# Kernel tuning notes

Hardware: AMD Instinct MI355X
Metric: run time of the kernel (lower is better)

The kernel has to match this reference:

```python
import jax, jax.numpy as jnp
import numpy as np

B, S, D, H, FB, K, FC = 16, 512, 256, 8, 128, 64, 32


def setup_inputs() -> dict:
    key = jax.random.key(0)
    ks = jax.random.split(key, 16)
    g = lambda i, shp: jax.random.normal(ks[i], shp, dtype=jnp.float32)
    inp = {
        "B_target": g(0, (B, S, FB)),
        "B_infected": g(1, (B, S, FB)),
        "E_target": g(2, (B, S, D)),
        "E_infected": g(3, (B, S, D)),
        "C_target": jax.random.uniform(ks[4], (B, S, K, FC), dtype=jnp.float32),
        "C_infected": jax.random.uniform(ks[5], (B, S, K, FC), dtype=jnp.float32),
        # learned parameters
        "W_bs": g(6, (FB, 1)) * 0.1,
        "W_cs": g(7, (FC, 1)) * 0.1,
        "W1": g(8, (H, D, D)) * (1.0 / np.sqrt(D)),  # per-head Attn W1, batched
        "W2": g(9, (H, D, D)) * (1.0 / np.sqrt(D)),
        "gamma_bs": jnp.ones((S,), jnp.float32),
        "beta_bs": jnp.zeros((S,), jnp.float32),
        "gamma_cs": jnp.ones((S,), jnp.float32),
        "beta_cs": jnp.zeros((S,), jnp.float32),
        "W_f": g(10, (2, 1)) * 0.1,
    }
    return inp


def _weighted_sum(x, W):
    # tf.nn.softmax over trailing size-1 axis of [F,1] -> all ones (faithful)
    return jnp.squeeze(x @ jax.nn.softmax(W, axis=-1), -1)


def _l2norm(x):
    return x * jax.lax.rsqrt(jnp.maximum(jnp.sum(x * x, -1, keepdims=True), 1e-12))


def _layernorm(x, gamma, beta, eps=1e-16):
    m = jnp.mean(x, -1, keepdims=True)
    v = jnp.mean(jnp.square(x - m), -1, keepdims=True)
    return (x - m) * jax.lax.rsqrt(v + eps) * gamma + beta


def _kld(y_true, y_pred, eps=1e-7):
    yt = jnp.clip(y_true, eps, 1.0)
    yp = jnp.clip(y_pred, eps, 1.0)
    return jnp.sum(yt * jnp.log(yt / yp), -1)


def _attn_br(Bvec, E, W1, W2):
    # batched multi-head version of the per-head Attn loop
    Q = jnp.einsum('bsd,hde->bhse', E, W1)
    Kh = jnp.einsum('bsd,hde->bhse', E, W2)
    scale = 1.0 / jnp.sqrt(jnp.asarray(E.shape[-1], E.dtype))
    scores = jnp.einsum('bhse,bhte->bhst', Q, Kh) * scale  # [b,H,S,S]
    A = jax.nn.softmax(scores, axis=2)  # original softmax(axis=1) on [b,S,S]
    # Dot(axes=(1,1)) of [b,S] with [b,S,S] -> [b,S]; stack heads, transpose -> [b,S,H]
    return jnp.einsum('bs,bhst->bth', Bvec, A)


def reference(B_target, B_infected, E_target, E_infected, C_target, C_infected,
              W_bs, W_cs, W1, W2, gamma_bs, beta_bs, gamma_cs, beta_cs, W_f):
    Bt = _weighted_sum(B_target, W_bs)   # [b,S]
    Bi = _weighted_sum(B_infected, W_bs)
    BR_t = _attn_br(Bt, E_target, W1, W2)    # [b,S,H]
    BR_i = _attn_br(Bi, E_infected, W1, W2)
    # keras CosineSimilarity loss = -cos_sim
    cos = -jnp.sum(_l2norm(BR_i) * _l2norm(BR_t), -1)  # [b,S]
    BS_out = _layernorm(cos, gamma_bs, beta_bs)
    Ct = _weighted_sum(C_target, W_cs)   # [b,S,K]
    Ci = _weighted_sum(C_infected, W_cs)
    Cm = 0.5 * (Ct + Ci)
    Cv = 0.5 * _kld(Ci, Cm) + 0.5 * _kld(Ct, Cm)  # [b,S]
    CS_out = _layernorm(Cv, gamma_cs, beta_cs)
    composite = jnp.stack([BS_out, CS_out], axis=-1)  # [b,S,2]
    out = jnp.squeeze(composite @ jax.nn.softmax(W_f, axis=-1), -1)
    return (out, BS_out, CS_out)
```

## Files before the change

kernel.cpp:

```cpp
#include <hip/hip_runtime.h>

#define NB 16
#define NS 512
#define ND 256
#define NH 8
#define NFB 128
#define NK 64
#define NFC 32

using f16 = _Float16;
using f16x4 = __attribute__((ext_vector_type(4))) f16;
using f16x8 = __attribute__((ext_vector_type(8))) f16;
using f32x4 = __attribute__((ext_vector_type(4))) float;

__device__ inline float waveReduceSum(float v) {
    #pragma unroll
    for (int off = 32; off; off >>= 1) v += __shfl_down(v, off);
    return v;
}

__device__ inline f32x4 mfma16(f16x8 a, f16x8 b, f32x4 c) {
    return __builtin_amdgcn_mfma_f32_16x16x32_f16(a, b, c, 0, 0, 0);
}

__global__ __launch_bounds__(256) void k_prep(const float* __restrict__ W1, const float* __restrict__ W2,
                                              f16* __restrict__ Mth,
                                              const float* __restrict__ Et_in, const float* __restrict__ Ei_in,
                                              f16* __restrict__ Ot, f16* __restrict__ Oi,
                                              const float* __restrict__ Bt_in, const float* __restrict__ Bi_in,
                                              float* __restrict__ Bt, float* __restrict__ Bi,
                                              const float* __restrict__ Ct, const float* __restrict__ Ci,
                                              float* __restrict__ Cv) {
    __shared__ float Wa[64][36];
    __shared__ float Wb[64][36];
    int bid = blockIdx.x;
    int tid = threadIdx.x;

    if (bid < 128) {
        int h  = bid >> 4;
        int j0 = ((bid >> 2) & 3) * 64;
        int i0 = (bid & 3) * 64;
        const float* A  = W2 + (size_t)h * ND * ND;
        const float* Bm = W1 + (size_t)h * ND * ND;
        int r = tid >> 4, c = tid & 15;
        float acc[4][4] = {};
        for (int d0 = 0; d0 < ND; d0 += 32) {
            __syncthreads();
            #pragma unroll
            for (int i = 0; i < 2; ++i) {
                int sid = tid + i * 256;
                int row = sid >> 3, seg = sid & 7;
                *(float4*)&Wa[row][seg * 4] = *(const float4*)&A [(size_t)(j0 + row) * ND + d0 + seg * 4];
                *(float4*)&Wb[row][seg * 4] = *(const float4*)&Bm[(size_t)(i0 + row) * ND + d0 + seg * 4];
            }
            __syncthreads();
            #pragma unroll 8
            for (int d = 0; d < 32; ++d) {
                float a0 = Wa[r*4+0][d], a1 = Wa[r*4+1][d], a2 = Wa[r*4+2][d], a3 = Wa[r*4+3][d];
                float b0 = Wb[c*4+0][d], b1 = Wb[c*4+1][d], b2 = Wb[c*4+2][d], b3 = Wb[c*4+3][d];
                acc[0][0] += a0*b0; acc[0][1] += a0*b1; acc[0][2] += a0*b2; acc[0][3] += a0*b3;
                acc[1][0] += a1*b0; acc[1][1] += a1*b1; acc[1][2] += a1*b2; acc[1][3] += a1*b3;
                acc[2][0] += a2*b0; acc[2][1] += a2*b1; acc[2][2] += a2*b2; acc[2][3] += a2*b3;
                acc[3][0] += a3*b0; acc[3][1] += a3*b1; acc[3][2] += a3*b2; acc[3][3] += a3*b3;
            }
        }
        #pragma unroll
        for (int a = 0; a < 4; ++a)
            #pragma unroll
            for (int bb = 0; bb < 4; ++bb)
                Mth[(size_t)h * ND * ND + (size_t)(j0 + r * 4 + a) * ND + (i0 + c * 4 + bb)] = (f16)acc[a][bb];
    } else if (bid < 128 + 4096) {
        const int n4 = NB * NS * ND / 4;
        int i = (bid - 128) * 256 + tid;
        const float* src; f16* dst;
        if (i < n4) { src = Et_in; dst = Ot; }
        else        { src = Ei_in; dst = Oi; i -= n4; }
        float4 v = ((const float4*)src)[i];
        f16x4 o = { (f16)v.x, (f16)v.y, (f16)v.z, (f16)v.w };
        ((f16x4*)dst)[i] = o;
    } else if (bid < 128 + 8192) {
        int wid = ((bid - 128 - 4096) * 256 + tid) >> 6;
        int lane = tid & 63;
        const float* src; float* dst; int row;
        if (wid < NB * NS) { src = Bt_in; dst = Bt; row = wid; }
        else               { src = Bi_in; dst = Bi; row = wid - NB * NS; }
        float2 v = ((const float2*)(src + (size_t)row * NFB))[lane];
        float s = waveReduceSum(v.x + v.y);
        if (lane == 0) dst[row] = s;
    } else {
        int gw = ((bid - 128 - 8192) * 256 + tid) >> 6;
        int lane = tid & 63;
        const float* pt = Ct + ((size_t)gw * NK + lane) * NFC;
        const float* pi = Ci + ((size_t)gw * NK + lane) * NFC;
        float st = 0.f, si = 0.f;
        #pragma unroll
        for (int j = 0; j < NFC; j += 4) {
            float4 vt = *(const float4*)(pt + j); st += vt.x + vt.y + vt.z + vt.w;
            float4 vi = *(const float4*)(pi + j); si += vi.x + vi.y + vi.z + vi.w;
        }
        float cm = 0.5f * (st + si);
        float yp = fminf(fmaxf(cm, 1e-7f), 1.0f);
        float y1 = fminf(fmaxf(si, 1e-7f), 1.0f);
        float y2 = fminf(fmaxf(st, 1e-7f), 1.0f);
        float term = 0.5f * (y1 * logf(y1 / yp) + y2 * logf(y2 / yp));
        term = waveReduceSum(term);
        if (lane == 0) Cv[gw] = term;
    }
}

__global__ __launch_bounds__(256, 2)
void k_attn4(const f16* __restrict__ Eft, const f16* __restrict__ Efi,
             const f16* __restrict__ Mth,
             const float* __restrict__ Bst, const float* __restrict__ Bsi,
             float* __restrict__ PEt, float* __restrict__ PBt,
             float* __restrict__ PEi, float* __restrict__ PBi) {
    int x = blockIdx.x;
    const f16* E; const float* Bvg; float *PE, *PB;
    if (x < 512) { E = Eft; Bvg = Bst; PE = PEt; PB = PBt; }
    else         { x -= 512; E = Efi; Bvg = Bsi; PE = PEi; PB = PBi; }
    int b = x >> 5, h = (x >> 2) & 7;
    int s0 = (x & 3) * 128;
    const f16* Ebase = E + (size_t)b * NS * ND;
    const f16* Mh = Mth + (size_t)h * ND * ND;
    float* PEo = PE + (size_t)(b * NH + h) * NS;
    float* PBo = PB + (size_t)(b * NH + h) * NS;

    __shared__ f16 smem[2 * 64 * 264];
    __shared__ float pe_s[NS], pb_s[NS];

    int tid = threadIdx.x;
    int lane = tid & 63, w = tid >> 6;
    int l16 = lane & 15, ch = lane >> 4;

    pe_s[tid] = 0.f; pe_s[tid + 256] = 0.f;
    pb_s[tid] = 0.f; pb_s[tid + 256] = 0.f;

    int sw0 = s0 + w * 32;

    f16x8 af[2][8];
    #pragma unroll
    for (int st = 0; st < 2; ++st) {
        f16x8 ebf[8];
        #pragma unroll
        for (int ki = 0; ki < 8; ++ki)
            ebf[ki] = *(const f16x8*)&Ebase[(size_t)(sw0 + st * 16 + l16) * ND + ki * 32 + ch * 8];

        #pragma unroll
        for (int jc = 0; jc < 8; ++jc) {
            __syncthreads();
            #pragma unroll
            for (int it = 0; it < 4; ++it) {
                int sid = tid + it * 256;
                int row = sid >> 5, seg = sid & 31;
                *(int4*)&smem[row * 264 + seg * 8] = *(const int4*)&Mh[(size_t)(jc * 32 + row) * ND + seg * 8];
            }
            __syncthreads();
            f32x4 acc[2] = {};
            #pragma unroll
            for (int ki = 0; ki < 8; ++ki) {
                f16x8 a0 = *(const f16x8*)&smem[(l16)      * 264 + ki * 32 + ch * 8];
                f16x8 a1 = *(const f16x8*)&smem[(16 + l16) * 264 + ki * 32 + ch * 8];
                acc[0] = mfma16(a0, ebf[ki], acc[0]);
                acc[1] = mfma16(a1, ebf[ki], acc[1]);
            }
            f16x8 vv;
            #pragma unroll
            for (int r = 0; r < 4; ++r) { vv[r] = (f16)acc[0][r]; vv[4 + r] = (f16)acc[1][r]; }
            af[st][jc] = vv;
        }
    }
    __syncthreads();

    float bvr[2][4];
    #pragma unroll
    for (int st = 0; st < 2; ++st)
        #pragma unroll
        for (int r = 0; r < 4; ++r)
            bvr[st][r] = Bvg[b * NS + sw0 + st * 16 + 4 * ch + r];

    int4 v[8];
    #pragma unroll
    for (int i = 0; i < 8; ++i) {
        int sid = tid + i * 256;
        int row = sid >> 5, seg = sid & 31;
        v[i] = *(const int4*)&Ebase[(size_t)row * ND + seg * 8];
    }
    #pragma unroll
    for (int i = 0; i < 8; ++i) {
        int sid = tid + i * 256;
        int row = sid >> 5, seg = sid & 31;
        *(int4*)&smem[row * 264 + seg * 8] = v[i];
    }

    for (int t = 0; t < 8; ++t) {
        f16* cur = smem + (t & 1) * (64 * 264);
        f16* nxt = smem + ((t + 1) & 1) * (64 * 264);
        if (t < 7) {
            int t0n = (t + 1) * 64;
            #pragma unroll
            for (int i = 0; i < 8; ++i) {
                int sid = tid + i * 256;
                int row = sid >> 5, seg = sid & 31;
                v[i] = *(const int4*)&Ebase[(size_t)(t0n + row) * ND + seg * 8];
            }
        }
        __syncthreads();
        int t0 = t * 64;
        f32x4 sacc[2][4] = {};
        #pragma unroll
        for (int kk = 0; kk < 8; ++kk)
            #pragma unroll
            for (int nt = 0; nt < 4; ++nt) {
                const f16* ep = &cur[(nt * 16 + l16) * 264 + kk * 32 + 4 * ch];
                f16x4 lo = *(const f16x4*)ep;
                f16x4 hi = *(const f16x4*)(ep + 16);
                f16x8 bf = { lo[0], lo[1], lo[2], lo[3], hi[0], hi[1], hi[2], hi[3] };
                sacc[0][nt] = mfma16(af[0][kk], bf, sacc[0][nt]);
                sacc[1][nt] = mfma16(af[1][kk], bf, sacc[1][nt]);
            }
        if (t < 7) {
            #pragma unroll
            for (int i = 0; i < 8; ++i) {
                int sid = tid + i * 256;
                int row = sid >> 5, seg = sid & 31;
                *(int4*)&nxt[row * 264 + seg * 8] = v[i];
            }
        }
        #pragma unroll
        for (int nt = 0; nt < 4; ++nt) {
            float se = 0.f, sw = 0.f;
            #pragma unroll
            for (int st = 0; st < 2; ++st)
                #pragma unroll
                for (int r = 0; r < 4; ++r) {
                    float e = __expf(sacc[st][nt][r] * 0.0625f);
                    se += e; sw += bvr[st][r] * e;
                }
            se += __shfl_down(se, 32); se += __shfl_down(se, 16);
            sw += __shfl_down(sw, 32); sw += __shfl_down(sw, 16);
            if (ch == 0) {
                atomicAdd(&pe_s[t0 + nt * 16 + l16], se);
                atomicAdd(&pb_s[t0 + nt * 16 + l16], sw);
            }
        }
    }
    __syncthreads();
    atomicAdd(&PEo[tid],       pe_s[tid]);
    atomicAdd(&PEo[tid + 256], pe_s[tid + 256]);
    atomicAdd(&PBo[tid],       pb_s[tid]);
    atomicAdd(&PBo[tid + 256], pb_s[tid + 256]);
}

__device__ inline float blockSum512(float v, float* rbuf) {
    v = waveReduceSum(v);
    int lane = threadIdx.x & 63, w = threadIdx.x >> 6;
    __syncthreads();
    if (lane == 0) rbuf[w] = v;
    __syncthreads();
    float s = 0.f;
    #pragma unroll
    for (int i = 0; i < 8; ++i) s += rbuf[i];
    return s;
}

__global__ __launch_bounds__(512) void k_final(const float* __restrict__ PEt, const float* __restrict__ PBt,
                                               const float* __restrict__ PEi, const float* __restrict__ PBi,
                                               const float* __restrict__ Cv,
                                               const float* __restrict__ gbs, const float* __restrict__ bbs,
                                               const float* __restrict__ gcs, const float* __restrict__ bcs,
                                               float* __restrict__ out) {
    __shared__ float rbuf[8];
    int b = blockIdx.x, s = threadIdx.x;
    float dot = 0.f, nt = 0.f, nu = 0.f;
    #pragma unroll
    for (int h = 0; h < NH; ++h) {
        size_t idx = (size_t)(b * NH + h) * NS + s;
        float tv = PBt[idx] / PEt[idx];
        float iv = PBi[idx] / PEi[idx];
        dot += tv * iv; nt += tv * tv; nu += iv * iv;
    }
    float cosv = -(dot * rsqrtf(fmaxf(nt, 1e-12f)) * rsqrtf(fmaxf(nu, 1e-12f)));

    float mc = blockSum512(cosv, rbuf) * (1.f / 512.f);
    float dc = cosv - mc;
    float vc = blockSum512(dc * dc, rbuf) * (1.f / 512.f);
    float BS = dc * rsqrtf(vc + 1e-16f) * gbs[s] + bbs[s];

    float cv = Cv[(size_t)b * NS + s];
    float mv = blockSum512(cv, rbuf) * (1.f / 512.f);
    float dv = cv - mv;
    float vv = blockSum512(dv * dv, rbuf) * (1.f / 512.f);
    float CS = dv * rsqrtf(vv + 1e-16f) * gcs[s] + bcs[s];

    out[(size_t)b * NS + s] = BS + CS;
    out[(size_t)NB * NS + (size_t)b * NS + s] = BS;
    out[(size_t)2 * NB * NS + (size_t)b * NS + s] = CS;
}

extern "C" void kernel_launch(void* const* d_in, const int* in_sizes, int n_in,
                              void* d_out, int out_size, void* d_ws, size_t ws_size,
                              hipStream_t stream) {
    const float* B_target   = (const float*)d_in[0];
    const float* B_infected = (const float*)d_in[1];
    const float* E_target   = (const float*)d_in[2];
    const float* E_infected = (const float*)d_in[3];
    const float* C_target   = (const float*)d_in[4];
    const float* C_infected = (const float*)d_in[5];
    const float* W1  = (const float*)d_in[8];
    const float* W2  = (const float*)d_in[9];
    const float* gbs = (const float*)d_in[10];
    const float* bbs = (const float*)d_in[11];
    const float* gcs = (const float*)d_in[12];
    const float* bcs = (const float*)d_in[13];
    float* out = (float*)d_out;

    char* ws = (char*)d_ws;
    size_t off = 0;
    auto alloc = [&](size_t n) { char* p = ws + off; off = (off + n + 255) & ~(size_t)255; return p; };
    float* Bt  = (float*)alloc((size_t)NB * NS * 4);
    float* Bi  = (float*)alloc((size_t)NB * NS * 4);
    float* Cv  = (float*)alloc((size_t)NB * NS * 4);
    float* PEt = (float*)alloc((size_t)NB * NH * NS * 4);
    float* PBt = (float*)alloc((size_t)NB * NH * NS * 4);
    float* PEi = (float*)alloc((size_t)NB * NH * NS * 4);
    float* PBi = (float*)alloc((size_t)NB * NH * NS * 4);
    f16* Mth = (f16*)alloc((size_t)NH * ND * ND * 2);
    f16* Eft = (f16*)alloc((size_t)NB * NS * ND * 2);
    f16* Efi = (f16*)alloc((size_t)NB * NS * ND * 2);

    hipMemsetAsync(PEt, 0, (size_t)4 * NB * NH * NS * 4, stream);
    k_prep<<<128 + 8192 + 2048, 256, 0, stream>>>(W1, W2, Mth,
                                                  E_target, E_infected, Eft, Efi,
                                                  B_target, B_infected, Bt, Bi,
                                                  C_target, C_infected, Cv);
    k_attn4<<<1024, 256, 0, stream>>>(Eft, Efi, Mth, Bt, Bi, PEt, PBt, PEi, PBi);
    k_final<<<NB, 512, 0, stream>>>(PEt, PBt, PEi, PBi, Cv, gbs, bbs, gcs, bcs, out);
}
```

Measured before the change: 328.0 us.

## Stage tiles via direct global-to-LDS loads with swizzle, drop atomics and memset

Replaces register-staged LDS tile loads in the attention kernel with global_load_lds direct copies into XOR-swizzled, unpadded double buffers. The tiles shrink to 32 rows, so LDS use drops and the launch bound asks for 4 blocks per CU. Per-chunk partial sums are now written to separate slots and reduced in the final kernel instead of using global atomics, which also removes the memset. This aims to cut register pressure, LDS traffic and atomic contention, at the cost of extra syncs per tile and more partial-buffer reads in the final kernel.

Measured after the change: 349.0 us. +6.4%, slower.

```diff
diff --git a/kernel.cpp b/kernel.cpp
--- a/kernel.cpp
+++ b/kernel.cpp
@@ -21,6 +21,12 @@
 
 __device__ inline f32x4 mfma16(f16x8 a, f16x8 b, f32x4 c) {
     return __builtin_amdgcn_mfma_f32_16x16x32_f16(a, b, c, 0, 0, 0);
+}
+
+__device__ inline void gload16(const void* g, void* l) {
+    __builtin_amdgcn_global_load_lds(
+        (const __attribute__((address_space(1))) void*)g,
+        (__attribute__((address_space(3))) void*)l, 16, 0, 0);
 }
 
 __global__ __launch_bounds__(256) void k_prep(const float* __restrict__ W1, const float* __restrict__ W2,
@@ -108,7 +114,7 @@
     }
 }
 
-__global__ __launch_bounds__(256, 2)
+__global__ __launch_bounds__(256, 4)
 void k_attn4(const f16* __restrict__ Eft, const f16* __restrict__ Efi,
              const f16* __restrict__ Mth,
              const float* __restrict__ Bst, const float* __restrict__ Bsi,
@@ -119,57 +125,70 @@
     if (x < 512) { E = Eft; Bvg = Bst; PE = PEt; PB = PBt; }
     else         { x -= 512; E = Efi; Bvg = Bsi; PE = PEi; PB = PBi; }
     int b = x >> 5, h = (x >> 2) & 7;
-    int s0 = (x & 3) * 128;
-    const f16* Ebase = E + (size_t)b * NS * ND;
-    const f16* Mh = Mth + (size_t)h * ND * ND;
-    float* PEo = PE + (size_t)(b * NH + h) * NS;
-    float* PBo = PB + (size_t)(b * NH + h) * NS;
-
-    __shared__ f16 smem[2 * 64 * 264];
+    int sc = x & 3;
+    int s0 = sc * 128;
+    const char* EbaseB = (const char*)(E + (size_t)b * NS * ND);
+    const char* MhB    = (const char*)(Mth + (size_t)h * ND * ND);
+    float* PEo = PE + (size_t)((b * NH + h) * 4 + sc) * NS;
+    float* PBo = PB + (size_t)((b * NH + h) * 4 + sc) * NS;
+
+    __shared__ f16 buf0[32 * 256];
+    __shared__ f16 buf1[32 * 256];
     __shared__ float pe_s[NS], pb_s[NS];
 
     int tid = threadIdx.x;
     int lane = tid & 63, w = tid >> 6;
     int l16 = lane & 15, ch = lane >> 4;
+    int swz = (l16 & 7) << 3;
 
     pe_s[tid] = 0.f; pe_s[tid + 256] = 0.f;
     pb_s[tid] = 0.f; pb_s[tid + 256] = 0.f;
 
     int sw0 = s0 + w * 32;
 
+    auto stage = [&](const char* matB, int row0, f16* buf) {
+        #pragma unroll
+        for (int i = 0; i < 4; ++i) {
+            int chunk = w * 4 + i;
+            int r = chunk * 2 + (lane >> 5);
+            int pcol = (lane & 31) * 16;
+            const char* src = matB + (size_t)(row0 + r) * 512 + (pcol ^ ((r & 7) << 4));
+            gload16(src, buf + chunk * 512 + lane * 8);
+        }
+    };
+
     f16x8 af[2][8];
     #pragma unroll
     for (int st = 0; st < 2; ++st) {
         f16x8 ebf[8];
         #pragma unroll
         for (int ki = 0; ki < 8; ++ki)
-            ebf[ki] = *(const f16x8*)&Ebase[(size_t)(sw0 + st * 16 + l16) * ND + ki * 32 + ch * 8];
-
+            ebf[ki] = *(const f16x8*)(EbaseB + (size_t)(sw0 + st * 16 + l16) * 512 + ki * 64 + ch * 16);
+
+        stage(MhB, 0, buf0);
+        __syncthreads();
         #pragma unroll
         for (int jc = 0; jc < 8; ++jc) {
+            f16* cur = (jc & 1) ? buf1 : buf0;
+            f16* nxt = (jc & 1) ? buf0 : buf1;
+            if (jc < 7) stage(MhB, (jc + 1) * 32, nxt);
+            f32x4 acc0 = {}, acc1 = {};
+            #pragma unroll
+            for (int ki = 0; ki < 8; ++ki) {
+                int c = (ki * 32 + ch * 8) ^ swz;
+                f16x8 a0 = *(const f16x8*)&cur[l16 * 256 + c];
+                f16x8 a1 = *(const f16x8*)&cur[(16 + l16) * 256 + c];
+                acc0 = mfma16(a0, ebf[ki], acc0);
+                acc1 = mfma16(a1, ebf[ki], acc1);
+            }
+            f16x8 vv;
+            #pragma unroll
+            for (int r = 0; r < 4; ++r) { vv[r] = (f16)acc0[r]; vv[4 + r] = (f16)acc1[r]; }
+            af[st][jc] = vv;
             __syncthreads();
-            #pragma unroll
-            for (int it = 0; it < 4; ++it) {
-                int sid = tid + it * 256;
-                int row = sid >> 5, seg = sid & 31;
-                *(int4*)&smem[row * 264 + seg * 8] = *(const int4*)&Mh[(size_t)(jc * 32 + row) * ND + seg * 8];
-            }
-            __syncthreads();
-            f32x4 acc[2] = {};
-            #pragma unroll
-            for (int ki = 0; ki < 8; ++ki) {
-                f16x8 a0 = *(const f16x8*)&smem[(l16)      * 264 + ki * 32 + ch * 8];
-                f16x8 a1 = *(const f16x8*)&smem[(16 + l16) * 264 + ki * 32 + ch * 8];
-                acc[0] = mfma16(a0, ebf[ki], acc[0]);
-                acc[1] = mfma16(a1, ebf[ki], acc[1]);
-            }
-            f16x8 vv;
-            #pragma unroll
-            for (int r = 0; r < 4; ++r) { vv[r] = (f16)acc[0][r]; vv[4 + r] = (f16)acc[1][r]; }
-            af[st][jc] = vv;
-        }
+        }
+        __builtin_amdgcn_sched_barrier(0);
     }
-    __syncthreads();
 
     float bvr[2][4];
     #pragma unroll
@@ -178,56 +197,30 @@
         for (int r = 0; r < 4; ++r)
             bvr[st][r] = Bvg[b * NS + sw0 + st * 16 + 4 * ch + r];
 
-    int4 v[8];
-    #pragma unroll
-    for (int i = 0; i < 8; ++i) {
-        int sid = tid + i * 256;
-        int row = sid >> 5, seg = sid & 31;
-        v[i] = *(const int4*)&Ebase[(size_t)row * ND + seg * 8];
-    }
-    #pragma unroll
-    for (int i = 0; i < 8; ++i) {
-        int sid = tid + i * 256;
-        int row = sid >> 5, seg = sid & 31;
-        *(int4*)&smem[row * 264 + seg * 8] = v[i];
-    }
-
-    for (int t = 0; t < 8; ++t) {
-        f16* cur = smem + (t & 1) * (64 * 264);
-        f16* nxt = smem + ((t + 1) & 1) * (64 * 264);
-        if (t < 7) {
-            int t0n = (t + 1) * 64;
-            #pragma unroll
-            for (int i = 0; i < 8; ++i) {
-                int sid = tid + i * 256;
-                int row = sid >> 5, seg = sid & 31;
-                v[i] = *(const int4*)&Ebase[(size_t)(t0n + row) * ND + seg * 8];
-            }
-        }
-        __syncthreads();
-        int t0 = t * 64;
-        f32x4 sacc[2][4] = {};
+    stage(EbaseB, 0, buf0);
+    __syncthreads();
+    #pragma unroll
+    for (int t = 0; t < 16; ++t) {
+        f16* cur = (t & 1) ? buf1 : buf0;
+        f16* nxt = (t & 1) ? buf0 : buf1;
+        if (t < 15) stage(EbaseB, (t + 1) * 32, nxt);
+        f32x4 sacc[2][2] = {};
         #pragma unroll
         for (int kk = 0; kk < 8; ++kk)
             #pragma unroll
-            for (int nt = 0; nt < 4; ++nt) {
-                const f16* ep = &cur[(nt * 16 + l16) * 264 + kk * 32 + 4 * ch];
-                f16x4 lo = *(const f16x4*)ep;
-                f16x4 hi = *(const f16x4*)(ep + 16);
+            for (int nt = 0; nt < 2; ++nt) {
+                int c0 = (kk * 32 + 4 * ch) ^ swz;
+                int c1 = (kk * 32 + 4 * ch + 16) ^ swz;
+                const f16* rowp = &cur[(nt * 16 + l16) * 256];
+                f16x4 lo = *(const f16x4*)(rowp + c0);
+                f16x4 hi = *(const f16x4*)(rowp + c1);
                 f16x8 bf = { lo[0], lo[1], lo[2], lo[3], hi[0], hi[1], hi[2], hi[3] };
                 sacc[0][nt] = mfma16(af[0][kk], bf, sacc[0][nt]);
                 sacc[1][nt] = mfma16(af[1][kk], bf, sacc[1][nt]);
             }
-        if (t < 7) {
-            #pragma unroll
-            for (int i = 0; i < 8; ++i) {
-                int sid = tid + i * 256;
-                int row = sid >> 5, seg = sid & 31;
-                *(int4*)&nxt[row * 264 + seg * 8] = v[i];
-            }
-        }
-        #pragma unroll
-        for (int nt = 0; nt < 4; ++nt) {
+        int t0 = t * 32;
+        #pragma unroll
+        for (int nt = 0; nt < 2; ++nt) {
             float se = 0.f, sw = 0.f;
             #pragma unroll
             for (int st = 0; st < 2; ++st)
@@ -243,12 +236,13 @@
                 atomicAdd(&pb_s[t0 + nt * 16 + l16], sw);
             }
         }
+        __syncthreads();
     }
-    __syncthreads();
-    atomicAdd(&PEo[tid],       pe_s[tid]);
-    atomicAdd(&PEo[tid + 256], pe_s[tid + 256]);
-    atomicAdd(&PBo[tid],       pb_s[tid]);
-    atomicAdd(&PBo[tid + 256], pb_s[tid + 256]);
+
+    PEo[tid]       = pe_s[tid];
+    PEo[tid + 256] = pe_s[tid + 256];
+    PBo[tid]       = pb_s[tid];
+    PBo[tid + 256] = pb_s[tid + 256];
 }
 
 __device__ inline float blockSum512(float v, float* rbuf) {
@@ -274,9 +268,15 @@
     float dot = 0.f, nt = 0.f, nu = 0.f;
     #pragma unroll
     for (int h = 0; h < NH; ++h) {
-        size_t idx = (size_t)(b * NH + h) * NS + s;
-        float tv = PBt[idx] / PEt[idx];
-        float iv = PBi[idx] / PEi[idx];
+        float pet = 0.f, pbt = 0.f, pei = 0.f, pbi = 0.f;
+        #pragma unroll
+        for (int sc = 0; sc < 4; ++sc) {
+            size_t idx = (size_t)((b * NH + h) * 4 + sc) * NS + s;
+            pet += PEt[idx]; pbt += PBt[idx];
+            pei += PEi[idx]; pbi += PBi[idx];
+        }
+        float tv = pbt / pet;
+        float iv = pbi / pei;
         dot += tv * iv; nt += tv * tv; nu += iv * iv;
     }
     float cosv = -(dot * rsqrtf(fmaxf(nt, 1e-12f)) * rsqrtf(fmaxf(nu, 1e-12f)));
@@ -320,15 +320,14 @@
     float* Bt  = (float*)alloc((size_t)NB * NS * 4);
     float* Bi  = (float*)alloc((size_t)NB * NS * 4);
     float* Cv  = (float*)alloc((size_t)NB * NS * 4);
-    float* PEt = (float*)alloc((size_t)NB * NH * NS * 4);
-    float* PBt = (float*)alloc((size_t)NB * NH * NS * 4);
-    float* PEi = (float*)alloc((size_t)NB * NH * NS * 4);
-    float* PBi = (float*)alloc((size_t)NB * NH * NS * 4);
+    float* PEt = (float*)alloc((size_t)NB * NH * 4 * NS * 4);
+    float* PBt = (float*)alloc((size_t)NB * NH * 4 * NS * 4);
+    float* PEi = (float*)alloc((size_t)NB * NH * 4 * NS * 4);
+    float* PBi = (float*)alloc((size_t)NB * NH * 4 * NS * 4);
     f16* Mth = (f16*)alloc((size_t)NH * ND * ND * 2);
     f16* Eft = (f16*)alloc((size_t)NB * NS * ND * 2);
     f16* Efi = (f16*)alloc((size_t)NB * NS * ND * 2);
 
-    hipMemsetAsync(PEt, 0, (size_t)4 * NB * NH * NS * 4, stream);
     k_prep<<<128 + 8192 + 2048, 256, 0, stream>>>(W1, W2, Mth,
                                                   E_target, E_infected, Eft, Efi,
                                                   B_target, B_infected, Bt, Bi,
```
